# Kernel optimization log

Hardware: AMD Instinct MI355X
Metric: run time of the kernel (lower is better)

Reference implementation:

```python
import jax, jax.numpy as jnp
import numpy as np

B, S, H, E, K = 2, 2048, 1024, 8, 2
CAP_FACTOR = 1.5

def setup_inputs() -> dict:
    key = jax.random.key(0)
    ks = jax.random.split(key, 8)
    sd1 = 1.0 / np.sqrt(H)
    sd2 = 1.0 / np.sqrt(H + E)
    return {
        'hidden_states': jax.random.normal(ks[0], (B, S, H), dtype=jnp.float32),
        'w1': jax.random.normal(ks[1], (H, H), dtype=jnp.float32) * sd1,
        'b1': jnp.zeros((H,), jnp.float32),
        'w2': jax.random.normal(ks[2], (H, E), dtype=jnp.float32) * sd1,
        'b2': jnp.zeros((E,), jnp.float32),
        'wc1': jax.random.normal(ks[3], (H + E, H), dtype=jnp.float32) * sd2,
        'bc1': jnp.zeros((H,), jnp.float32),
        'wc2': jax.random.normal(ks[4], (H, E), dtype=jnp.float32) * sd1,
        'bc2': jnp.zeros((E,), jnp.float32),
        'cache_hit_rates': jax.random.uniform(ks[5], (E,), dtype=jnp.float32),
    }

def reference(hidden_states, w1, b1, w2, b2, wc1, bc1, wc2, bc2, cache_hit_rates):
    b, s, h = hidden_states.shape
    # router MLP: Linear -> ReLU -> Linear
    router_logits = jax.nn.relu(hidden_states @ w1 + b1) @ w2 + b2  # [B,S,E]
    # cache-aware adjustment
    avg_features = hidden_states.mean(axis=1)  # [B,H]
    combined = jnp.concatenate(
        [avg_features, jnp.broadcast_to(cache_hit_rates[None, :], (b, E))], axis=-1)
    adj = jnp.tanh(jax.nn.relu(combined @ wc1 + bc1) @ wc2 + bc2)  # [B,E]
    router_logits = router_logits + adj[:, None, :]
    router_probs = jax.nn.softmax(router_logits, axis=-1)  # [B,S,E]
    top_k_probs, top_k_indices = jax.lax.top_k(router_probs, K)  # [B,S,K]
    top_k_probs = top_k_probs / (top_k_probs.sum(axis=-1, keepdims=True) + 1e-8)
    capacity = int(b * s * CAP_FACTOR * K / E)
    # flatten in (b, s, k) order to replicate serial capacity counters
    N = b * s * K
    e_flat = top_k_indices.reshape(N)
    p_flat = top_k_probs.reshape(N)
    tok = jnp.arange(N) // K  # token index b*S+s
    onehot = jax.nn.one_hot(e_flat, E, dtype=jnp.int32)  # [N,E] small
    prior = jnp.cumsum(onehot, axis=0) - onehot  # exclusive count per expert
    pos = prior[jnp.arange(N), e_flat]  # slot within expert
    keep = pos < capacity
    posc = jnp.minimum(pos, capacity - 1)
    val = keep.astype(router_probs.dtype)
    dispatch = jnp.zeros((b * s, E, capacity), router_probs.dtype)
    dispatch = dispatch.at[tok, e_flat, posc].add(val).reshape(b, s, E, capacity)
    combine = jnp.zeros((b * s, E, capacity), router_probs.dtype)
    combine = combine.at[tok, e_flat, posc].add(val * p_flat).reshape(b, s, E, capacity)
    # load balancing aux loss
    router_prob_per_expert = router_probs.mean(axis=(0, 1))  # [E]
    expert_usage_rate = onehot.astype(router_probs.dtype).mean(axis=0)  # [E]
    aux_loss = jnp.sum(router_prob_per_expert * expert_usage_rate) * E
    return dispatch, combine, router_probs, aux_loss
```

## Files before the change

### kernel.cpp

```cpp
#include <hip/hip_runtime.h>
#include <hip/hip_bf16.h>

#define BB 2
#define SS 2048
#define HH 1024
#define EE 8
#define KK 2
#define CAP 1536
#define NTOK (BB * SS)
#define NASSIGN (NTOK * KK)

#define WS_PSUM   0
#define WS_AVG    8
#define WS_HC     2056
#define WS_ADJ    4104
#define WS_P1     4120
#define WS_P2     8216
#define WS_IDX    12312
#define WS_LOGITS 16408
#define WS_ZERO_FLOATS 4112
#define WS_ZERO_BYTES 16448
#define WS_BF16_BYTE 196704
#define WS_H_BYTE (WS_BF16_BYTE + 31457280)
#define WS_NEED (WS_H_BYTE + 16777216ull)

using short8 = __attribute__((ext_vector_type(8))) short;
using u16x8  = __attribute__((ext_vector_type(8))) unsigned short;
using f32x4  = __attribute__((ext_vector_type(4))) float;

__device__ __forceinline__ unsigned short f2bf(float f) {
  unsigned u = __float_as_uint(f);
  unsigned r = (u + 0x7fffu + ((u >> 16) & 1u)) >> 16;
  return (unsigned short)r;
}
__device__ __forceinline__ float bf2f(unsigned short h) {
  return __uint_as_float((unsigned)h << 16);
}
__device__ __forceinline__ void split3(float x, unsigned short& h,
                                       unsigned short& m, unsigned short& l) {
  h = f2bf(x);
  float r = x - bf2f(h);
  m = f2bf(r);
  l = f2bf(r - bf2f(m));
}

__device__ __forceinline__ void gload_lds16(const void* g, void* l) {
  __builtin_amdgcn_global_load_lds(
      (const __attribute__((address_space(1))) void*)g,
      (__attribute__((address_space(3))) void*)l, 16, 0, 0);
}

#define PREPX_BLKS 4096
#define PREPW_BLKS 256
#define AVG_BLKS   128
__global__ __launch_bounds__(256) void k_prep(
    const float* __restrict__ x, const float* __restrict__ w1,
    unsigned short* __restrict__ Xh, unsigned short* __restrict__ Xm,
    unsigned short* __restrict__ Xl,
    unsigned short* __restrict__ Wh, unsigned short* __restrict__ Wm,
    unsigned short* __restrict__ Wl,
    float* __restrict__ wshead, float* __restrict__ avg_part) {
  __shared__ unsigned short Th[64 * 65], Tm[64 * 65], Tl[64 * 65];
  int tid = threadIdx.x;
  int bid = blockIdx.x;
  if (bid < PREPX_BLKS) {
    if (bid == 0)
      for (int j = tid; j < WS_ZERO_FLOATS; j += 256) wshead[j] = 0.f;
    int i = (bid * 256 + tid) * 4;
    float4 v = *(const float4*)&x[i];
    unsigned short h[4], m[4], l[4];
    split3(v.x, h[0], m[0], l[0]);
    split3(v.y, h[1], m[1], l[1]);
    split3(v.z, h[2], m[2], l[2]);
    split3(v.w, h[3], m[3], l[3]);
    *(ushort4*)&Xh[i] = make_ushort4(h[0], h[1], h[2], h[3]);
    *(ushort4*)&Xm[i] = make_ushort4(m[0], m[1], m[2], m[3]);
    *(ushort4*)&Xl[i] = make_ushort4(l[0], l[1], l[2], l[3]);
  } else if (bid < PREPX_BLKS + PREPW_BLKS) {
    int pid = bid - PREPX_BLKS;
    int k0 = (pid & 15) * 64, n0 = (pid >> 4) * 64;
    for (int i = 0; i < 16; ++i) {
      int e = i * 256 + tid;
      int k = e >> 6, n = e & 63;
      float v = w1[(size_t)(k0 + k) * HH + n0 + n];
      unsigned short h, m, l;
      split3(v, h, m, l);
      Th[n * 65 + k] = h; Tm[n * 65 + k] = m; Tl[n * 65 + k] = l;
    }
    __syncthreads();
    for (int i = 0; i < 16; ++i) {
      int e = i * 256 + tid;
      int n = e >> 6, k = e & 63;
      size_t o = (size_t)(n0 + n) * HH + k0 + k;
      Wh[o] = Th[n * 65 + k]; Wm[o] = Tm[n * 65 + k]; Wl[o] = Tl[n * 65 + k];
    }
  } else {
    int pid = bid - PREPX_BLKS - PREPW_BLKS;
    int h = (pid & 3) * 256 + tid;
    int c = (pid >> 2) & 15;
    int b = pid >> 6;
    const float* p = x + (size_t)b * SS * HH + (size_t)(c * 128) * HH + h;
    float s = 0.f;
    for (int i = 0; i < 128; ++i) s += p[(size_t)i * HH];
    avg_part[(c * BB + b) * HH + h] = s;
  }
}

__global__ void k_avgp(const float* __restrict__ x, float* __restrict__ avg_part) {
  int h = blockIdx.x * 256 + threadIdx.x;
  int c = blockIdx.y;
  int b = blockIdx.z;
  const float* p = x + (size_t)b * SS * HH + (size_t)(c * 128) * HH + h;
  float s = 0.f;
  for (int i = 0; i < 128; ++i) s += p[(size_t)i * HH];
  avg_part[(c * BB + b) * HH + h] = s;
}

__global__ void k_hc(const float* __restrict__ avg_part, const float* __restrict__ chr,
                     const float* __restrict__ wc1, float* __restrict__ hc_raw) {
  __shared__ float avg_s[128];
  int tid = threadIdx.x;
  int j = blockIdx.x * 256 + tid;
  int c = blockIdx.y;
  int b = blockIdx.z;
  if (tid < 128) {
    float s = 0.f;
    for (int cc = 0; cc < 16; ++cc)
      s += avg_part[(cc * BB + b) * HH + c * 128 + tid];
    avg_s[tid] = s * (1.0f / SS);
  }
  __syncthreads();
  float acc = 0.f;
  for (int il = 0; il < 128; ++il)
    acc += avg_s[il] * wc1[(size_t)(c * 128 + il) * HH + j];
  if (c == 7)
    for (int i = 0; i < EE; ++i)
      acc += chr[i] * wc1[(size_t)(HH + i) * HH + j];
  atomicAdd(&hc_raw[b * HH + j], acc);
}

__global__ void k_adj(const float* __restrict__ hc_raw, const float* __restrict__ bc1,
                      const float* __restrict__ wc2, const float* __restrict__ bc2,
                      float* __restrict__ adj) {
  int b = blockIdx.x;
  int tid = threadIdx.x;
  float part[EE] = {};
  for (int j = tid; j < HH; j += 256) {
    float v = fmaxf(hc_raw[b * HH + j] + bc1[j], 0.f);
    for (int e = 0; e < EE; ++e) part[e] += v * wc2[j * EE + e];
  }
  for (int m = 1; m < 64; m <<= 1)
    for (int e = 0; e < EE; ++e) part[e] += __shfl_xor(part[e], m);
  __shared__ float red[4][EE];
  int wave = tid >> 6, lane = tid & 63;
  if (lane == 0)
    for (int e = 0; e < EE; ++e) red[wave][e] = part[e];
  __syncthreads();
  if (tid < EE) {
    float s = bc2[tid];
    for (int w = 0; w < 4; ++w) s += red[w][tid];
    adj[b * EE + tid] = tanhf(s);
  }
}

#define BM 128
#define BN 64
#define BK 32
#define ZF4_PER_BLOCK 49152
__global__ __launch_bounds__(256) void k_gemm_mfma(
    const unsigned short* __restrict__ Xh, const unsigned short* __restrict__ Xm,
    const unsigned short* __restrict__ Xl,
    const unsigned short* __restrict__ Wh, const unsigned short* __restrict__ Wm,
    const unsigned short* __restrict__ Wl,
    const float* __restrict__ b1, float* __restrict__ hbuf,
    f32x4* __restrict__ zout,
    const float* __restrict__ hc_raw, const float* __restrict__ bc1,
    const float* __restrict__ wc2, const float* __restrict__ bc2,
    float* __restrict__ adj) {
  __shared__ unsigned short As[3][BM * BK];
  __shared__ unsigned short Bs[3][BN * BK];
  __shared__ float b1s[BN];
  __shared__ float red[4][EE];
  int tid = threadIdx.x;

  if (blockIdx.y == HH / BN) {
    if (blockIdx.x >= BB) return;
    int b = blockIdx.x;
    float part[EE] = {};
    for (int j = tid; j < HH; j += 256) {
      float v = fmaxf(hc_raw[b * HH + j] + bc1[j], 0.f);
      for (int e = 0; e < EE; ++e) part[e] += v * wc2[j * EE + e];
    }
    for (int m = 1; m < 64; m <<= 1)
      for (int e = 0; e < EE; ++e) part[e] += __shfl_xor(part[e], m);
    int wave = tid >> 6, lane = tid & 63;
    if (lane == 0)
      for (int e = 0; e < EE; ++e) red[wave][e] = part[e];
    __syncthreads();
    if (tid < EE) {
      float s = bc2[tid];
      for (int w = 0; w < 4; ++w) s += red[w][tid];
      adj[b * EE + tid] = tanhf(s);
    }
    return;
  }

  int m0 = blockIdx.x * BM, n0 = blockIdx.y * BN;
  if (tid < BN) b1s[tid] = b1[n0 + tid];

  int bid = blockIdx.y * gridDim.x + blockIdx.x;
  f32x4* zp = zout + (size_t)bid * ZF4_PER_BLOCK;
  const f32x4 z4 = {0.f, 0.f, 0.f, 0.f};

  int lane = tid & 63, wave = tid >> 6;
  int wm = wave & 1, wn = wave >> 1;
  int q = lane >> 4, mr = lane & 15;
  int lr = lane >> 2, lq = lane & 3;

  f32x4 acc[4][2] = {};

  const unsigned short* Ag[3] = {Xh, Xm, Xl};
  const unsigned short* Bg[3] = {Wh, Wm, Wl};

  for (int k0 = 0; k0 < HH; k0 += BK) {
    __syncthreads();
#pragma unroll
    for (int j = 0; j < 6; ++j) {
      int i = wave + 4 * j;
      int s = i >> 3, g = i & 7;
      const unsigned short* gp =
          Ag[s] + (size_t)(m0 + g * 16 + lr) * HH + k0 + lq * 8;
      gload_lds16(gp, &As[s][g * 512]);
    }
#pragma unroll
    for (int j = 0; j < 3; ++j) {
      int i = wave + 4 * j;
      int s = i >> 2, g = i & 3;
      const unsigned short* gp =
          Bg[s] + (size_t)(n0 + g * 16 + lr) * HH + k0 + lq * 8;
      gload_lds16(gp, &Bs[s][g * 512]);
    }
    __syncthreads();

    {
      int ki = k0 >> 5;
      f32x4* zb = zp + ki * (256 * 6) + tid;
#pragma unroll
      for (int j = 0; j < 6; ++j) __builtin_nontemporal_store(z4, &zb[j * 256]);
    }

    short8 af[3][4], bf[3][2];
#pragma unroll
    for (int s = 0; s < 3; ++s) {
#pragma unroll
      for (int mi = 0; mi < 4; ++mi)
        af[s][mi] = *(const short8*)&As[s][(wm * 64 + mi * 16 + mr) * BK + q * 8];
#pragma unroll
      for (int ni = 0; ni < 2; ++ni)
        bf[s][ni] = *(const short8*)&Bs[s][(wn * 32 + ni * 16 + mr) * BK + q * 8];
    }
#pragma unroll
    for (int mi = 0; mi < 4; ++mi)
#pragma unroll
      for (int ni = 0; ni < 2; ++ni) {
        f32x4 c = acc[mi][ni];
        c = __builtin_amdgcn_mfma_f32_16x16x32_bf16(af[0][mi], bf[0][ni], c, 0, 0, 0);
        c = __builtin_amdgcn_mfma_f32_16x16x32_bf16(af[0][mi], bf[1][ni], c, 0, 0, 0);
        c = __builtin_amdgcn_mfma_f32_16x16x32_bf16(af[1][mi], bf[0][ni], c, 0, 0, 0);
        c = __builtin_amdgcn_mfma_f32_16x16x32_bf16(af[0][mi], bf[2][ni], c, 0, 0, 0);
        c = __builtin_amdgcn_mfma_f32_16x16x32_bf16(af[2][mi], bf[0][ni], c, 0, 0, 0);
        c = __builtin_amdgcn_mfma_f32_16x16x32_bf16(af[1][mi], bf[1][ni], c, 0, 0, 0);
        acc[mi][ni] = c;
      }
  }

#pragma unroll
  for (int ni = 0; ni < 2; ++ni) {
    int cloc = wn * 32 + ni * 16 + mr;
    int col = n0 + cloc;
    float bv = b1s[cloc];
#pragma unroll
    for (int mi = 0; mi < 4; ++mi)
#pragma unroll
      for (int r = 0; r < 4; ++r) {
        int row = m0 + wm * 64 + mi * 16 + q * 4 + r;
        hbuf[(size_t)row * HH + col] = fmaxf(acc[mi][ni][r] + bv, 0.f);
      }
  }
}

__global__ __launch_bounds__(256) void k_logits(
    const float* __restrict__ h, const float* __restrict__ w2,
    const float* __restrict__ b2, const float* __restrict__ adj,
    float* __restrict__ probs_out, int* __restrict__ idx_pack,
    float* __restrict__ p1o, float* __restrict__ p2o, float* __restrict__ psum) {
  __shared__ float w2s[HH * EE];
  __shared__ float ps[EE];
  int tid = threadIdx.x;
#pragma unroll
  for (int j = 0; j < 8; ++j)
    ((float4*)w2s)[tid + 256 * j] = ((const float4*)w2)[tid + 256 * j];
  if (tid < EE) ps[tid] = 0.f;
  __syncthreads();

  int lane = tid & 63, wave = tid >> 6;
  int t = blockIdx.x * 4 + wave;
  float acc[EE] = {};
  const float* hr = h + (size_t)t * HH;
#pragma unroll
  for (int i = 0; i < 16; ++i) {
    int e = lane + 64 * i;
    float hv = hr[e];
    float4 wa = ((const float4*)w2s)[2 * e];
    float4 wb = ((const float4*)w2s)[2 * e + 1];
    acc[0] += hv * wa.x; acc[1] += hv * wa.y; acc[2] += hv * wa.z; acc[3] += hv * wa.w;
    acc[4] += hv * wb.x; acc[5] += hv * wb.y; acc[6] += hv * wb.z; acc[7] += hv * wb.w;
  }
#pragma unroll
  for (int m = 1; m < 64; m <<= 1)
#pragma unroll
    for (int e = 0; e < EE; ++e) acc[e] += __shfl_xor(acc[e], m);

  if (lane == 0) {
    int b = t >> 11;
    float l[EE];
    float mx = -1e30f;
    for (int e = 0; e < EE; ++e) {
      l[e] = acc[e] + b2[e] + adj[b * EE + e];
      mx = fmaxf(mx, l[e]);
    }
    float s = 0.f;
    for (int e = 0; e < EE; ++e) { l[e] = expf(l[e] - mx); s += l[e]; }
    float inv = 1.f / s;
    for (int e = 0; e < EE; ++e) { l[e] *= inv; probs_out[t * EE + e] = l[e]; }
    int e1 = 0; float p1 = l[0];
    for (int e = 1; e < EE; ++e) if (l[e] > p1) { p1 = l[e]; e1 = e; }
    int e2 = -1; float p2 = -1.f;
    for (int e = 0; e < EE; ++e) if (e != e1 && l[e] > p2) { p2 = l[e]; e2 = e; }
    float norm = 1.f / (p1 + p2 + 1e-8f);
    idx_pack[t] = e1 | (e2 << 8);
    p1o[t] = p1 * norm;
    p2o[t] = p2 * norm;
    for (int e = 0; e < EE; ++e) atomicAdd(&ps[e], l[e]);
  }
  __syncthreads();
  if (tid < EE) atomicAdd(&psum[tid], ps[tid]);
}

__global__ __launch_bounds__(256) void k_gemm_f32(
    const float* __restrict__ X, const float* __restrict__ w1,
    const float* __restrict__ b1, const float* __restrict__ w2,
    float* __restrict__ logits) {
  __shared__ float Asf[16][65];
  __shared__ float Bsf[16][64];
  __shared__ float w2sf[64][EE];
  int tid = threadIdx.x;
  int m0 = blockIdx.x * 64, n0 = blockIdx.y * 64;
  for (int i = tid; i < 64 * EE; i += 256)
    w2sf[i / EE][i % EE] = w2[(size_t)(n0 + i / EE) * EE + (i % EE)];
  float acc[4][4] = {};
  int tx = tid & 15, ty = tid >> 4;
  for (int k0 = 0; k0 < HH; k0 += 16) {
    for (int idx = tid; idx < 64 * 16; idx += 256) {
      int m = idx >> 4, kk = idx & 15;
      Asf[kk][m] = X[(size_t)(m0 + m) * HH + k0 + kk];
    }
    for (int idx = tid; idx < 16 * 64; idx += 256) {
      int kk = idx >> 6, n = idx & 63;
      Bsf[kk][n] = w1[(size_t)(k0 + kk) * HH + n0 + n];
    }
    __syncthreads();
    for (int kk = 0; kk < 16; ++kk) {
      float a[4], bb[4];
      for (int i = 0; i < 4; ++i) a[i] = Asf[kk][ty * 4 + i];
      for (int j = 0; j < 4; ++j) bb[j] = Bsf[kk][tx * 4 + j];
      for (int i = 0; i < 4; ++i)
        for (int j = 0; j < 4; ++j) acc[i][j] += a[i] * bb[j];
    }
    __syncthreads();
  }
  float p[4][EE] = {};
  for (int i = 0; i < 4; ++i)
    for (int j = 0; j < 4; ++j) {
      int c = tx * 4 + j;
      float v = fmaxf(acc[i][j] + b1[n0 + c], 0.f);
      for (int e = 0; e < EE; ++e) p[i][e] += v * w2sf[c][e];
    }
  for (int m = 1; m < 16; m <<= 1)
    for (int i = 0; i < 4; ++i)
      for (int e = 0; e < EE; ++e) p[i][e] += __shfl_xor(p[i][e], m);
  if (tx == 0)
    for (int i = 0; i < 4; ++i)
      for (int e = 0; e < EE; ++e)
        atomicAdd(&logits[(size_t)(m0 + ty * 4 + i) * EE + e], p[i][e]);
}

__global__ void k_init_logits(const float* __restrict__ adj, const float* __restrict__ b2,
                              float* __restrict__ logits) {
  int i = blockIdx.x * 256 + threadIdx.x;
  int e = i & 7;
  int t = i >> 3;
  int b = t >> 11;
  logits[i] = b2[e] + adj[b * EE + e];
}

__global__ void k_softmax(const float* __restrict__ logits, float* __restrict__ probs_out,
                          int* __restrict__ idx_pack, float* __restrict__ p1o,
                          float* __restrict__ p2o, float* __restrict__ psum) {
  int t = blockIdx.x * 256 + threadIdx.x;
  float l[EE];
  float mx = -1e30f;
  for (int e = 0; e < EE; ++e) { l[e] = logits[t * EE + e]; mx = fmaxf(mx, l[e]); }
  float s = 0.f;
  for (int e = 0; e < EE; ++e) { l[e] = expf(l[e] - mx); s += l[e]; }
  float inv = 1.f / s;
  for (int e = 0; e < EE; ++e) { l[e] *= inv; probs_out[t * EE + e] = l[e]; }
  int e1 = 0; float p1 = l[0];
  for (int e = 1; e < EE; ++e) if (l[e] > p1) { p1 = l[e]; e1 = e; }
  int e2 = -1; float p2 = -1.f;
  for (int e = 0; e < EE; ++e) if (e != e1 && l[e] > p2) { p2 = l[e]; e2 = e; }
  float norm = 1.f / (p1 + p2 + 1e-8f);
  idx_pack[t] = e1 | (e2 << 8);
  p1o[t] = p1 * norm;
  p2o[t] = p2 * norm;
  for (int m = 1; m < 64; m <<= 1)
    for (int e = 0; e < EE; ++e) l[e] += __shfl_xor(l[e], m);
  if ((threadIdx.x & 63) == 0)
    for (int e = 0; e < EE; ++e) atomicAdd(&psum[e], l[e]);
}

__global__ __launch_bounds__(256) void k_route(
    const int* __restrict__ idx_pack, const float* __restrict__ p1,
    const float* __restrict__ p2, const float* __restrict__ psum,
    float* __restrict__ disp, float* __restrict__ comb, float* __restrict__ aux_out) {
  __shared__ int cnt[256][EE];
  __shared__ int tot[EE];
  int tid = threadIdx.x;
  const int CH = NASSIGN / 256;
  int n0 = tid * CH;
  int local[EE] = {};
  for (int n = n0; n < n0 + CH; ++n) {
    int t = n >> 1;
    int pk = idx_pack[t];
    int e = (n & 1) ? (pk >> 8) : (pk & 0xff);
    local[e]++;
  }
  for (int e = 0; e < EE; ++e) cnt[tid][e] = local[e];
  __syncthreads();
  if (tid < EE) {
    int run = 0;
    for (int t = 0; t < 256; ++t) { int v = cnt[t][tid]; cnt[t][tid] = run; run += v; }
    tot[tid] = run;
  }
  __syncthreads();
  int off[EE];
  for (int e = 0; e < EE; ++e) off[e] = cnt[tid][e];
  for (int n = n0; n < n0 + CH; ++n) {
    int t = n >> 1;
    int pk = idx_pack[t];
    int e; float p;
    if (n & 1) { e = pk >> 8; p = p2[t]; } else { e = pk & 0xff; p = p1[t]; }
    int pos = off[e]++;
    if (pos < CAP) {
      size_t o = (size_t)t * EE * CAP + (size_t)e * CAP + pos;
      disp[o] = 1.0f;
      comb[o] = p;
    }
  }
  if (tid == 0) {
    float aux = 0.f;
    for (int e = 0; e < EE; ++e)
      aux += (psum[e] / (float)NTOK) * ((float)tot[e] / (float)NASSIGN);
    aux_out[0] = aux * (float)EE;
  }
}

extern "C" void kernel_launch(void* const* d_in, const int* in_sizes, int n_in,
                              void* d_out, int out_size, void* d_ws, size_t ws_size,
                              hipStream_t stream) {
  const float* x   = (const float*)d_in[0];
  const float* w1  = (const float*)d_in[1];
  const float* b1  = (const float*)d_in[2];
  const float* w2  = (const float*)d_in[3];
  const float* b2  = (const float*)d_in[4];
  const float* wc1 = (const float*)d_in[5];
  const float* bc1 = (const float*)d_in[6];
  const float* wc2 = (const float*)d_in[7];
  const float* bc2 = (const float*)d_in[8];
  const float* chr = (const float*)d_in[9];

  float* out = (float*)d_out;
  float* disp  = out;
  float* comb  = disp + (size_t)NTOK * EE * CAP;
  float* probs = comb + (size_t)NTOK * EE * CAP;
  float* aux   = probs + (size_t)NTOK * EE;

  float* ws = (float*)d_ws;
  float* psum   = ws + WS_PSUM;
  float* hcr    = ws + WS_HC;
  float* adj    = ws + WS_ADJ;
  float* p1     = ws + WS_P1;
  float* p2     = ws + WS_P2;
  int*   idxp   = (int*)(ws + WS_IDX);
  float* logits = ws + WS_LOGITS;
  float* avgp   = ws + WS_LOGITS;

  char* wsb = (char*)d_ws;
  unsigned short* Xh = (unsigned short*)(wsb + WS_BF16_BYTE);
  unsigned short* Xm = Xh + (size_t)NTOK * HH;
  unsigned short* Xl = Xm + (size_t)NTOK * HH;
  unsigned short* Wh = Xl + (size_t)NTOK * HH;
  unsigned short* Wm = Wh + (size_t)HH * HH;
  unsigned short* Wl = Wm + (size_t)HH * HH;
  float* hbuf = (float*)(wsb + WS_H_BYTE);

  bool use_mfma = ws_size >= WS_NEED;

  if (use_mfma) {
    k_prep<<<PREPX_BLKS + PREPW_BLKS + AVG_BLKS, 256, 0, stream>>>(
        x, w1, Xh, Xm, Xl, Wh, Wm, Wl, ws, avgp);
    k_hc<<<dim3(HH / 256, 8, BB), 256, 0, stream>>>(avgp, chr, wc1, hcr);
    k_gemm_mfma<<<dim3(NTOK / BM, HH / BN + 1), 256, 0, stream>>>(
        Xh, Xm, Xl, Wh, Wm, Wl, b1, hbuf, (f32x4*)d_out,
        hcr, bc1, wc2, bc2, adj);
    k_logits<<<NTOK / 4, 256, 0, stream>>>(hbuf, w2, b2, adj, probs, idxp, p1, p2, psum);
  } else {
    hipMemsetAsync(d_ws, 0, WS_ZERO_BYTES, stream);
    hipMemsetAsync(d_out, 0, (size_t)out_size * sizeof(float), stream);
    k_avgp<<<dim3(HH / 256, 16, BB), 256, 0, stream>>>(x, avgp);
    k_hc<<<dim3(HH / 256, 8, BB), 256, 0, stream>>>(avgp, chr, wc1, hcr);
    k_adj<<<BB, 256, 0, stream>>>(hcr, bc1, wc2, bc2, adj);
    k_init_logits<<<(NTOK * EE) / 256, 256, 0, stream>>>(adj, b2, logits);
    k_gemm_f32<<<dim3(NTOK / 64, HH / 64), 256, 0, stream>>>(x, w1, b1, w2, logits);
    k_softmax<<<NTOK / 256, 256, 0, stream>>>(logits, probs, idxp, p1, p2, psum);
    k_route<<<1, 256, 0, stream>>>(idxp, p1, p2, psum, disp, comb, aux);
  }
  if (use_mfma)
    k_route<<<1, 256, 0, stream>>>(idxp, p1, p2, psum, disp, comb, aux);
}
```

Baseline: 511.7 us.

## Fuse second router linear into MFMA GEMM epilogue and double-buffer LDS

The second linear layer (h @ w2) moves into the GEMM epilogue. Each block reduces its 64-column slice against w2 and atomically adds partial logits per token, so the 16 MB hidden buffer is no longer written or re-read. The K loop now double-buffers LDS, and output zeroing moves into dedicated blocks instead of being spread across GEMM iterations. GEMM tiles are swizzled across the grid, and a lightweight per-token softmax kernel replaces the old logits kernel. In exchange it adds float atomics, whose summation order is non-deterministic, and doubles LDS use, which can lower occupancy.

Measured after the change: 691.0 us. +35.0%, slower.

```diff
diff --git a/kernel.cpp b/kernel.cpp
--- a/kernel.cpp
+++ b/kernel.cpp
@@ -59,13 +59,18 @@
     unsigned short* __restrict__ Xl,
     unsigned short* __restrict__ Wh, unsigned short* __restrict__ Wm,
     unsigned short* __restrict__ Wl,
-    float* __restrict__ wshead, float* __restrict__ avg_part) {
+    float* __restrict__ wshead, float* __restrict__ avg_part,
+    float* __restrict__ lgz) {
   __shared__ unsigned short Th[64 * 65], Tm[64 * 65], Tl[64 * 65];
   int tid = threadIdx.x;
   int bid = blockIdx.x;
   if (bid < PREPX_BLKS) {
     if (bid == 0)
       for (int j = tid; j < WS_ZERO_FLOATS; j += 256) wshead[j] = 0.f;
+    if (bid >= 1 && bid <= 32) {
+      const float4 z = {0.f, 0.f, 0.f, 0.f};
+      ((float4*)lgz)[(bid - 1) * 256 + tid] = z;
+    }
     int i = (bid * 256 + tid) * 4;
     float4 v = *(const float4*)&x[i];
     unsigned short h[4], m[4], l[4];
@@ -166,26 +171,37 @@
 #define BM 128
 #define BN 64
 #define BK 32
-#define ZF4_PER_BLOCK 49152
-__global__ __launch_bounds__(256) void k_gemm_mfma(
+#define NZBLK 64
+#define NZF4 393216
+#define NGEMM 512
+__global__ __launch_bounds__(256) void k_fused(
     const unsigned short* __restrict__ Xh, const unsigned short* __restrict__ Xm,
     const unsigned short* __restrict__ Xl,
     const unsigned short* __restrict__ Wh, const unsigned short* __restrict__ Wm,
     const unsigned short* __restrict__ Wl,
-    const float* __restrict__ b1, float* __restrict__ hbuf,
+    const float* __restrict__ b1, const float* __restrict__ w2,
     f32x4* __restrict__ zout,
     const float* __restrict__ hc_raw, const float* __restrict__ bc1,
     const float* __restrict__ wc2, const float* __restrict__ bc2,
-    float* __restrict__ adj) {
-  __shared__ unsigned short As[3][BM * BK];
-  __shared__ unsigned short Bs[3][BN * BK];
+    float* __restrict__ adj, float* __restrict__ logits) {
+  __shared__ unsigned short As[2][3][BM * BK];
+  __shared__ unsigned short Bs[2][3][BN * BK];
   __shared__ float b1s[BN];
+  __shared__ float w2s[BN * 9];
   __shared__ float red[4][EE];
   int tid = threadIdx.x;
-
-  if (blockIdx.y == HH / BN) {
-    if (blockIdx.x >= BB) return;
-    int b = blockIdx.x;
+  int bid = blockIdx.x;
+
+  if (bid < NZBLK) {
+    f32x4* zb = zout + (size_t)bid * NZF4 + tid;
+    const f32x4 z4 = {0.f, 0.f, 0.f, 0.f};
+#pragma unroll 8
+    for (int j = 0; j < NZF4 / 256; ++j)
+      __builtin_nontemporal_store(z4, &zb[(size_t)j * 256]);
+    return;
+  }
+  if (bid < NZBLK + BB) {
+    int b = bid - NZBLK;
     float part[EE] = {};
     for (int j = tid; j < HH; j += 256) {
       float v = fmaxf(hc_raw[b * HH + j] + bc1[j], 0.f);
@@ -205,12 +221,17 @@
     return;
   }
 
-  int m0 = blockIdx.x * BM, n0 = blockIdx.y * BN;
+  int g = bid - NZBLK - BB;
+  int gs = (g & 7) * 64 + (g >> 3);
+  int m0 = (gs >> 4) * BM, n0 = (gs & 15) * BN;
+
   if (tid < BN) b1s[tid] = b1[n0 + tid];
-
-  int bid = blockIdx.y * gridDim.x + blockIdx.x;
-  f32x4* zp = zout + (size_t)bid * ZF4_PER_BLOCK;
-  const f32x4 z4 = {0.f, 0.f, 0.f, 0.f};
+#pragma unroll
+  for (int rdx = 0; rdx < 2; ++rdx) {
+    int i = tid + rdx * 256;
+    int c = i >> 3, e = i & 7;
+    w2s[c * 9 + e] = w2[(size_t)(n0 + c) * EE + e];
+  }
 
   int lane = tid & 63, wave = tid >> 6;
   int wm = wave & 1, wn = wave >> 1;
@@ -218,133 +239,126 @@
   int lr = lane >> 2, lq = lane & 3;
 
   f32x4 acc[4][2] = {};
-
   const unsigned short* Ag[3] = {Xh, Xm, Xl};
   const unsigned short* Bg[3] = {Wh, Wm, Wl};
 
-  for (int k0 = 0; k0 < HH; k0 += BK) {
-    __syncthreads();
+  auto STAGE = [&](int t, int bf) {
+    int k0 = t * BK;
 #pragma unroll
     for (int j = 0; j < 6; ++j) {
       int i = wave + 4 * j;
-      int s = i >> 3, g = i & 7;
-      const unsigned short* gp =
-          Ag[s] + (size_t)(m0 + g * 16 + lr) * HH + k0 + lq * 8;
-      gload_lds16(gp, &As[s][g * 512]);
+      int s = i >> 3, gg = i & 7;
+      gload_lds16(Ag[s] + (size_t)(m0 + gg * 16 + lr) * HH + k0 + lq * 8,
+                  &As[bf][s][gg * 512]);
     }
 #pragma unroll
     for (int j = 0; j < 3; ++j) {
       int i = wave + 4 * j;
-      int s = i >> 2, g = i & 3;
-      const unsigned short* gp =
-          Bg[s] + (size_t)(n0 + g * 16 + lr) * HH + k0 + lq * 8;
-      gload_lds16(gp, &Bs[s][g * 512]);
-    }
-    __syncthreads();
-
-    {
-      int ki = k0 >> 5;
-      f32x4* zb = zp + ki * (256 * 6) + tid;
-#pragma unroll
-      for (int j = 0; j < 6; ++j) __builtin_nontemporal_store(z4, &zb[j * 256]);
-    }
-
-    short8 af[3][4], bf[3][2];
+      int s = i >> 2, gg = i & 3;
+      gload_lds16(Bg[s] + (size_t)(n0 + gg * 16 + lr) * HH + k0 + lq * 8,
+                  &Bs[bf][s][gg * 512]);
+    }
+  };
+
+  STAGE(0, 0);
+  __syncthreads();
+  int cur = 0;
+  for (int t = 0; t < HH / BK; ++t) {
+    if (t + 1 < HH / BK) STAGE(t + 1, cur ^ 1);
+
+    short8 af[3][4], bv[3][2];
 #pragma unroll
     for (int s = 0; s < 3; ++s) {
 #pragma unroll
       for (int mi = 0; mi < 4; ++mi)
-        af[s][mi] = *(const short8*)&As[s][(wm * 64 + mi * 16 + mr) * BK + q * 8];
+        af[s][mi] = *(const short8*)&As[cur][s][(wm * 64 + mi * 16 + mr) * BK + q * 8];
 #pragma unroll
       for (int ni = 0; ni < 2; ++ni)
-        bf[s][ni] = *(const short8*)&Bs[s][(wn * 32 + ni * 16 + mr) * BK + q * 8];
+        bv[s][ni] = *(const short8*)&Bs[cur][s][(wn * 32 + ni * 16 + mr) * BK + q * 8];
     }
 #pragma unroll
     for (int mi = 0; mi < 4; ++mi)
 #pragma unroll
       for (int ni = 0; ni < 2; ++ni) {
         f32x4 c = acc[mi][ni];
-        c = __builtin_amdgcn_mfma_f32_16x16x32_bf16(af[0][mi], bf[0][ni], c, 0, 0, 0);
-        c = __builtin_amdgcn_mfma_f32_16x16x32_bf16(af[0][mi], bf[1][ni], c, 0, 0, 0);
-        c = __builtin_amdgcn_mfma_f32_16x16x32_bf16(af[1][mi], bf[0][ni], c, 0, 0, 0);
-        c = __builtin_amdgcn_mfma_f32_16x16x32_bf16(af[0][mi], bf[2][ni], c, 0, 0, 0);
-        c = __builtin_amdgcn_mfma_f32_16x16x32_bf16(af[2][mi], bf[0][ni], c, 0, 0, 0);
-        c = __builtin_amdgcn_mfma_f32_16x16x32_bf16(af[1][mi], bf[1][ni], c, 0, 0, 0);
+        c = __builtin_amdgcn_mfma_f32_16x16x32_bf16(af[0][mi], bv[0][ni], c, 0, 0, 0);
+        c = __builtin_amdgcn_mfma_f32_16x16x32_bf16(af[0][mi], bv[1][ni], c, 0, 0, 0);
+        c = __builtin_amdgcn_mfma_f32_16x16x32_bf16(af[1][mi], bv[0][ni], c, 0, 0, 0);
+        c = __builtin_amdgcn_mfma_f32_16x16x32_bf16(af[0][mi], bv[2][ni], c, 0, 0, 0);
+        c = __builtin_amdgcn_mfma_f32_16x16x32_bf16(af[2][mi], bv[0][ni], c, 0, 0, 0);
+        c = __builtin_amdgcn_mfma_f32_16x16x32_bf16(af[1][mi], bv[1][ni], c, 0, 0, 0);
         acc[mi][ni] = c;
       }
-  }
-
-#pragma unroll
-  for (int ni = 0; ni < 2; ++ni) {
-    int cloc = wn * 32 + ni * 16 + mr;
-    int col = n0 + cloc;
-    float bv = b1s[cloc];
-#pragma unroll
-    for (int mi = 0; mi < 4; ++mi)
-#pragma unroll
-      for (int r = 0; r < 4; ++r) {
-        int row = m0 + wm * 64 + mi * 16 + q * 4 + r;
-        hbuf[(size_t)row * HH + col] = fmaxf(acc[mi][ni][r] + bv, 0.f);
+    __syncthreads();
+    cur ^= 1;
+  }
+
+#pragma unroll
+  for (int mi = 0; mi < 4; ++mi)
+#pragma unroll
+    for (int r = 0; r < 4; ++r) {
+      int rowl = wm * 64 + mi * 16 + q * 4 + r;
+      int c0 = wn * 32 + mr, c1 = c0 + 16;
+      float v0 = fmaxf(acc[mi][0][r] + b1s[c0], 0.f);
+      float v1 = fmaxf(acc[mi][1][r] + b1s[c1], 0.f);
+      float pe[EE];
+#pragma unroll
+      for (int e = 0; e < EE; ++e)
+        pe[e] = v0 * w2s[c0 * 9 + e] + v1 * w2s[c1 * 9 + e];
+#pragma unroll
+      for (int m = 1; m < 16; m <<= 1)
+#pragma unroll
+        for (int e = 0; e < EE; ++e) pe[e] += __shfl_xor(pe[e], m);
+      if (mr == 0) {
+        float* lp = &logits[(size_t)(m0 + rowl) * EE];
+#pragma unroll
+        for (int e = 0; e < EE; ++e) atomicAdd(&lp[e], pe[e]);
       }
-  }
-}
-
-__global__ __launch_bounds__(256) void k_logits(
-    const float* __restrict__ h, const float* __restrict__ w2,
-    const float* __restrict__ b2, const float* __restrict__ adj,
-    float* __restrict__ probs_out, int* __restrict__ idx_pack,
-    float* __restrict__ p1o, float* __restrict__ p2o, float* __restrict__ psum) {
-  __shared__ float w2s[HH * EE];
-  __shared__ float ps[EE];
-  int tid = threadIdx.x;
-#pragma unroll
-  for (int j = 0; j < 8; ++j)
-    ((float4*)w2s)[tid + 256 * j] = ((const float4*)w2)[tid + 256 * j];
-  if (tid < EE) ps[tid] = 0.f;
-  __syncthreads();
-
-  int lane = tid & 63, wave = tid >> 6;
-  int t = blockIdx.x * 4 + wave;
-  float acc[EE] = {};
-  const float* hr = h + (size_t)t * HH;
-#pragma unroll
-  for (int i = 0; i < 16; ++i) {
-    int e = lane + 64 * i;
-    float hv = hr[e];
-    float4 wa = ((const float4*)w2s)[2 * e];
-    float4 wb = ((const float4*)w2s)[2 * e + 1];
-    acc[0] += hv * wa.x; acc[1] += hv * wa.y; acc[2] += hv * wa.z; acc[3] += hv * wa.w;
-    acc[4] += hv * wb.x; acc[5] += hv * wb.y; acc[6] += hv * wb.z; acc[7] += hv * wb.w;
-  }
+    }
+}
+
+__global__ __launch_bounds__(256) void k_softmax2(
+    const float* __restrict__ logits, const float* __restrict__ b2,
+    const float* __restrict__ adj, float* __restrict__ probs_out,
+    int* __restrict__ idx_pack, float* __restrict__ p1o, float* __restrict__ p2o,
+    float* __restrict__ psum) {
+  int t = blockIdx.x * 256 + threadIdx.x;
+  int b = t >> 11;
+  float4 la = *(const float4*)&logits[(size_t)t * EE];
+  float4 lb = *(const float4*)&logits[(size_t)t * EE + 4];
+  float l[EE] = {la.x, la.y, la.z, la.w, lb.x, lb.y, lb.z, lb.w};
+  float mx = -1e30f;
+#pragma unroll
+  for (int e = 0; e < EE; ++e) {
+    l[e] += b2[e] + adj[b * EE + e];
+    mx = fmaxf(mx, l[e]);
+  }
+  float s = 0.f;
+#pragma unroll
+  for (int e = 0; e < EE; ++e) { l[e] = expf(l[e] - mx); s += l[e]; }
+  float inv = 1.f / s;
+#pragma unroll
+  for (int e = 0; e < EE; ++e) l[e] *= inv;
+  float4 pa = {l[0], l[1], l[2], l[3]}, pb = {l[4], l[5], l[6], l[7]};
+  *(float4*)&probs_out[(size_t)t * EE] = pa;
+  *(float4*)&probs_out[(size_t)t * EE + 4] = pb;
+  int e1 = 0; float p1 = l[0];
+#pragma unroll
+  for (int e = 1; e < EE; ++e) if (l[e] > p1) { p1 = l[e]; e1 = e; }
+  int e2 = -1; float p2 = -1.f;
+#pragma unroll
+  for (int e = 0; e < EE; ++e) if (e != e1 && l[e] > p2) { p2 = l[e]; e2 = e; }
+  float norm = 1.f / (p1 + p2 + 1e-8f);
+  idx_pack[t] = e1 | (e2 << 8);
+  p1o[t] = p1 * norm;
+  p2o[t] = p2 * norm;
 #pragma unroll
   for (int m = 1; m < 64; m <<= 1)
 #pragma unroll
-    for (int e = 0; e < EE; ++e) acc[e] += __shfl_xor(acc[e], m);
-
-  if (lane == 0) {
-    int b = t >> 11;
-    float l[EE];
-    float mx = -1e30f;
-    for (int e = 0; e < EE; ++e) {
-      l[e] = acc[e] + b2[e] + adj[b * EE + e];
-      mx = fmaxf(mx, l[e]);
-    }
-    float s = 0.f;
-    for (int e = 0; e < EE; ++e) { l[e] = expf(l[e] - mx); s += l[e]; }
-    float inv = 1.f / s;
-    for (int e = 0; e < EE; ++e) { l[e] *= inv; probs_out[t * EE + e] = l[e]; }
-    int e1 = 0; float p1 = l[0];
-    for (int e = 1; e < EE; ++e) if (l[e] > p1) { p1 = l[e]; e1 = e; }
-    int e2 = -1; float p2 = -1.f;
-    for (int e = 0; e < EE; ++e) if (e != e1 && l[e] > p2) { p2 = l[e]; e2 = e; }
-    float norm = 1.f / (p1 + p2 + 1e-8f);
-    idx_pack[t] = e1 | (e2 << 8);
-    p1o[t] = p1 * norm;
-    p2o[t] = p2 * norm;
-    for (int e = 0; e < EE; ++e) atomicAdd(&ps[e], l[e]);
-  }
-  __syncthreads();
-  if (tid < EE) atomicAdd(&psum[tid], ps[tid]);
+    for (int e = 0; e < EE; ++e) l[e] += __shfl_xor(l[e], m);
+  if ((threadIdx.x & 63) == 0)
+#pragma unroll
+    for (int e = 0; e < EE; ++e) atomicAdd(&psum[e], l[e]);
 }
 
 __global__ __launch_bounds__(256) void k_gemm_f32(
@@ -512,18 +526,18 @@
   unsigned short* Wh = Xl + (size_t)NTOK * HH;
   unsigned short* Wm = Wh + (size_t)HH * HH;
   unsigned short* Wl = Wm + (size_t)HH * HH;
-  float* hbuf = (float*)(wsb + WS_H_BYTE);
+  float* lgz = (float*)(wsb + WS_H_BYTE);
 
   bool use_mfma = ws_size >= WS_NEED;
 
   if (use_mfma) {
     k_prep<<<PREPX_BLKS + PREPW_BLKS + AVG_BLKS, 256, 0, stream>>>(
-        x, w1, Xh, Xm, Xl, Wh, Wm, Wl, ws, avgp);
+        x, w1, Xh, Xm, Xl, Wh, Wm, Wl, ws, avgp, lgz);
     k_hc<<<dim3(HH / 256, 8, BB), 256, 0, stream>>>(avgp, chr, wc1, hcr);
-    k_gemm_mfma<<<dim3(NTOK / BM, HH / BN + 1), 256, 0, stream>>>(
-        Xh, Xm, Xl, Wh, Wm, Wl, b1, hbuf, (f32x4*)d_out,
-        hcr, bc1, wc2, bc2, adj);
-    k_logits<<<NTOK / 4, 256, 0, stream>>>(hbuf, w2, b2, adj, probs, idxp, p1, p2, psum);
+    k_fused<<<NZBLK + BB + NGEMM, 256, 0, stream>>>(
+        Xh, Xm, Xl, Wh, Wm, Wl, b1, w2, (f32x4*)d_out,
+        hcr, bc1, wc2, bc2, adj, lgz);
+    k_softmax2<<<NTOK / 256, 256, 0, stream>>>(lgz, b2, adj, probs, idxp, p1, p2, psum);
   } else {
     hipMemsetAsync(d_ws, 0, WS_ZERO_BYTES, stream);
     hipMemsetAsync(d_out, 0, (size_t)out_size * sizeof(float), stream);
@@ -533,8 +547,6 @@
     k_init_logits<<<(NTOK * EE) / 256, 256, 0, stream>>>(adj, b2, logits);
     k_gemm_f32<<<dim3(NTOK / 64, HH / 64), 256, 0, stream>>>(x, w1, b1, w2, logits);
     k_softmax<<<NTOK / 256, 256, 0, stream>>>(logits, probs, idxp, p1, p2, psum);
-    k_route<<<1, 256, 0, stream>>>(idxp, p1, p2, psum, disp, comb, aux);
-  }
-  if (use_mfma)
-    k_route<<<1, 256, 0, stream>>>(idxp, p1, p2, psum, disp, comb, aux);
-}
+  }
+  k_route<<<1, 256, 0, stream>>>(idxp, p1, p2, psum, disp, comb, aux);
+}
```
